# Optimization experiments

Hardware: AMD Instinct MI355X
Metric: run time of the kernel (lower is better)

The kernel has to match this reference:

```python
import jax, jax.numpy as jnp
import numpy as np

FEAT_DIM = 2048
H_DIM = 1024
N = 8192  # num_obj (tree nodes in pre-order traversal order)


def setup_inputs() -> dict:
    key = jax.random.key(0)
    ks = jax.random.split(key, 5)
    features = jax.random.normal(ks[0], (N, FEAT_DIM), dtype=jnp.float32)
    # block_orthogonal init approximated by scaled gaussian (same math at runtime)
    Wx = jax.random.normal(ks[1], (4 * H_DIM, FEAT_DIM), dtype=jnp.float32) / np.sqrt(FEAT_DIM)
    Wh = jax.random.normal(ks[2], (4 * H_DIM, H_DIM), dtype=jnp.float32) / np.sqrt(H_DIM)
    bx = jnp.zeros((4 * H_DIM,), dtype=jnp.float32)
    # iofuh bias: forget-gate block [2h:3h] filled with 1.0
    bh = jnp.zeros((4 * H_DIM,), dtype=jnp.float32).at[2 * H_DIM:3 * H_DIM].set(1.0)
    # binary tree in pre-order-compatible (topological) order: parent of t is (t-1)//2 < t; root = -1
    t = jnp.arange(N)
    parent_idx = jnp.where(t == 0, -1, (t - 1) // 2).astype(jnp.int32)
    root_c = jax.random.normal(ks[3], (1, H_DIM), dtype=jnp.float32)
    root_h = jax.random.normal(ks[4], (1, H_DIM), dtype=jnp.float32)
    return {"features": features, "Wx": Wx, "bx": bx, "Wh": Wh, "bh": bh,
            "parent_idx": parent_idx, "root_c": root_c, "root_h": root_h}


def reference(features, Wx, bx, Wh, bh, parent_idx, root_c, root_h):
    # Precompute the input projection for ALL nodes with one big GEMM
    # (the original does this per-node; math is identical).
    xproj = features @ Wx.T + (bx + bh)  # [N, 4H]
    WhT = Wh.T  # [H, 4H]
    # state buffers; slot 0 holds the root state, slot t+1 holds node t's state
    h_buf = jnp.concatenate([root_h, jnp.zeros((N, H_DIM), features.dtype)], axis=0)  # [N+1, H]
    c_buf = jnp.concatenate([root_c, jnp.zeros((N, H_DIM), features.dtype)], axis=0)

    def step(carry, inp):
        h_buf, c_buf = carry
        t, p, xp = inp
        hp = h_buf[p + 1]  # parent hidden [H]
        cp = c_buf[p + 1]  # parent cell   [H]
        iofu = xp + hp @ WhT  # [4H]
        i, o, f, u = jnp.split(iofu, 4)
        i = jax.nn.sigmoid(i)
        o = jax.nn.sigmoid(o)
        f = jax.nn.sigmoid(f)
        u = jnp.tanh(u)
        c = i * u + f * cp
        h = o * jnp.tanh(c)
        h_buf = h_buf.at[t + 1].set(h)
        c_buf = c_buf.at[t + 1].set(c)
        return (h_buf, c_buf), h

    ts = jnp.arange(N)
    (_, _), hidden = jax.lax.scan(step, (h_buf, c_buf), (ts, parent_idx, xproj))
    return hidden  # [N, H] == treelstm_io.hidden rows in traversal order
```

## Files before the change

kernel.cpp:

```cpp
#include <hip/hip_runtime.h>
#include <math.h>

#define FEAT 2048
#define HD 1024
#define FH 4096
#define NN 8192

using s16x8 = __attribute__((ext_vector_type(8))) short;
using f32x4 = __attribute__((ext_vector_type(4))) float;

#define GLOBAL_AS __attribute__((address_space(1)))
#define LDS_AS __attribute__((address_space(3)))

__device__ __forceinline__ void gload_lds16(const void* g, void* l) {
    __builtin_amdgcn_global_load_lds((const GLOBAL_AS unsigned int*)g,
                                     (LDS_AS unsigned int*)l, 16, 0, 0);
}

__device__ __forceinline__ unsigned short f2bf(float f) {
    union { float f; unsigned u; } v; v.f = f;
    unsigned r = v.u + 0x7FFFu + ((v.u >> 16) & 1u);
    return (unsigned short)(r >> 16);
}

__device__ __forceinline__ float fast_sig(float x) { return 1.0f / (1.0f + __expf(-x)); }
__device__ __forceinline__ float fast_tanh(float x) {
    float ax = fabsf(x);
    float e = __expf(2.0f * ax);
    float r = 1.0f - 2.0f / (e + 1.0f);
    return copysignf(r, x);
}

__global__ __launch_bounds__(256) void convert_all_kernel(
    const float* __restrict__ feat, const float* __restrict__ Wx,
    const float* __restrict__ Wh, unsigned short* __restrict__ feat_b,
    unsigned short* __restrict__ Wx_b, unsigned short* __restrict__ Wh_b)
{
    const size_t n1 = (size_t)NN * FEAT;
    const size_t n2 = n1 + (size_t)FH * FEAT;
    size_t i = ((size_t)blockIdx.x * 256 + threadIdx.x) * 8;
    const float* s; unsigned short* d;
    if (i < n1)      { s = feat + i;        d = feat_b + i; }
    else if (i < n2) { s = Wx + (i - n1);   d = Wx_b + (i - n1); }
    else             { s = Wh + (i - n2);   d = Wh_b + (i - n2); }
    float4 a = *(const float4*)s;
    float4 b = *(const float4*)(s + 4);
    unsigned short r[8] = {f2bf(a.x), f2bf(a.y), f2bf(a.z), f2bf(a.w),
                           f2bf(b.x), f2bf(b.y), f2bf(b.z), f2bf(b.w)};
    *(s16x8*)d = *(const s16x8*)r;
}

__global__ __launch_bounds__(256) void init_kernel(
    const float* __restrict__ root_h, const float* __restrict__ root_c,
    unsigned short* __restrict__ h_buf, float* __restrict__ c_buf)
{
    const int i = blockIdx.x * 256 + threadIdx.x;
    if (i < HD) { h_buf[i] = f2bf(root_h[i]); c_buf[i] = root_c[i]; }
}

__global__ __launch_bounds__(512, 2) void xproj_8ph(
    const unsigned short* __restrict__ Ab,
    const unsigned short* __restrict__ Bb,
    const float* __restrict__ bx, const float* __restrict__ bh,
    float* __restrict__ xproj)
{
    __shared__ char lds[131072];
    const int tid = threadIdx.x;
    const int wid = tid >> 6;
    const int lane = tid & 63;
    const int wr = wid >> 2;
    const int wc = wid & 3;
    const int bm = blockIdx.x * 256;
    const int bn = blockIdx.y * 256;
    const int fr = lane & 15;
    const int fq = lane >> 4;

    const int srow = tid >> 3;
    const int sslot = (tid & 7) ^ (srow & 7);
    const unsigned short* gA[4];
    const unsigned short* gB[4];
    #pragma unroll
    for (int q = 0; q < 4; ++q) {
        gA[q] = Ab + (size_t)(bm + q * 64 + srow) * FEAT + sslot * 8;
        gB[q] = Bb + (size_t)(bn + q * 64 + srow) * FEAT + sslot * 8;
    }
    const int ldsoff = tid * 16;

    f32x4 acc[8][4];
    #pragma unroll
    for (int i = 0; i < 8; ++i)
        #pragma unroll
        for (int j = 0; j < 4; ++j) { f32x4 z = {0.f, 0.f, 0.f, 0.f}; acc[i][j] = z; }

    #pragma unroll
    for (int q = 0; q < 4; ++q) {
        gload_lds16(gA[q], lds + q * 8192 + ldsoff);
        gload_lds16(gB[q], lds + 32768 + q * 8192 + ldsoff);
    }

    for (int t = 0; t < 32; ++t) {
        const int d = t & 1;
        const char* LA = lds + d * 65536;
        const char* LB = LA + 32768;
        char* SA = lds + (d ^ 1) * 65536;
        char* SB = SA + 32768;
        const int knext = (t + 1) * 64;

        asm volatile("s_waitcnt vmcnt(0)" ::: "memory");
        __builtin_amdgcn_s_barrier();

        #pragma unroll
        for (int kk = 0; kk < 2; ++kk) {
            const int kbyte = kk * 64 + fq * 16;
            s16x8 aF[8], bF[4];
            #pragma unroll
            for (int i = 0; i < 8; ++i) {
                const int row = wr * 128 + i * 16 + fr;
                aF[i] = *(const s16x8*)(LA + row * 128 + (kbyte ^ ((row & 7) << 4)));
            }
            #pragma unroll
            for (int j = 0; j < 4; ++j) {
                const int row = wc * 64 + j * 16 + fr;
                bF[j] = *(const s16x8*)(LB + row * 128 + (kbyte ^ ((row & 7) << 4)));
            }
            if (t < 31) {
                if (kk == 0) {
                    #pragma unroll
                    for (int q = 0; q < 4; ++q)
                        gload_lds16(gA[q] + knext, SA + q * 8192 + ldsoff);
                } else {
                    #pragma unroll
                    for (int q = 0; q < 4; ++q)
                        gload_lds16(gB[q] + knext, SB + q * 8192 + ldsoff);
                }
            }
            __builtin_amdgcn_s_setprio(1);
            #pragma unroll
            for (int i = 0; i < 8; ++i)
                #pragma unroll
                for (int j = 0; j < 4; ++j)
                    acc[i][j] = __builtin_amdgcn_mfma_f32_16x16x32_bf16(
                        aF[i], bF[j], acc[i][j], 0, 0, 0);
            __builtin_amdgcn_s_setprio(0);
        }
    }

    #pragma unroll
    for (int j = 0; j < 4; ++j) {
        const int col = bn + wc * 64 + j * 16 + fr;
        const float bias = bx[col] + bh[col];
        #pragma unroll
        for (int i = 0; i < 8; ++i) {
            const int rowb = bm + wr * 128 + i * 16 + fq * 4;
            #pragma unroll
            for (int reg = 0; reg < 4; ++reg)
                xproj[(size_t)(rowb + reg) * FH + col] = acc[i][j][reg] + bias;
        }
    }
}

template<int BM>
__global__ __launch_bounds__(512, 2) void level_kk(
    const float* __restrict__ xproj, const unsigned short* __restrict__ Whb,
    int start, int prevstart, unsigned short* __restrict__ h_buf,
    float* __restrict__ c_buf, float* __restrict__ out)
{
    constexpr int MR = BM / 32;
    constexpr int ABYTES = BM * 128;
    constexpr int BUF = ABYTES + 32768;
    __shared__ char lds[2 * BUF];
    const int tid = threadIdx.x;
    const int wid = tid >> 6, lane = tid & 63;
    const int wr = wid >> 2, wc = wid & 3;
    const int fr = lane & 15, fq = lane >> 4;
    const int t0 = start + blockIdx.x * BM;
    const int jg0 = blockIdx.y * 64;

    const int srow = tid >> 3;
    const int sslot = (tid & 7) ^ (srow & 7);
    const unsigned short* gA[BM / 64];
    #pragma unroll
    for (int q = 0; q < BM / 64; ++q) {
        const int rg = blockIdx.x * BM + q * 64 + srow;
        gA[q] = h_buf + (size_t)(prevstart + (rg >> 1) + 1) * HD + sslot * 8;
    }
    const unsigned short* gB[4];
    #pragma unroll
    for (int q = 0; q < 4; ++q) {
        const int r = q * 64 + srow;
        const int whrow = ((r >> 4) & 3) * 1024 + jg0 + ((r >> 6) * 16) + (r & 15);
        gB[q] = Whb + (size_t)whrow * HD + sslot * 8;
    }
    const int ldsoff = tid * 16;

    f32x4 acc[MR][4];
    #pragma unroll
    for (int i = 0; i < MR; ++i)
        #pragma unroll
        for (int j = 0; j < 4; ++j) { f32x4 z = {0.f, 0.f, 0.f, 0.f}; acc[i][j] = z; }

    #pragma unroll
    for (int q = 0; q < BM / 64; ++q)
        gload_lds16(gA[q], lds + q * 8192 + ldsoff);
    #pragma unroll
    for (int q = 0; q < 4; ++q)
        gload_lds16(gB[q], lds + ABYTES + q * 8192 + ldsoff);

    for (int t = 0; t < 16; ++t) {
        const char* LA = lds + (t & 1) * BUF;
        const char* LB = LA + ABYTES;
        char* SA = lds + ((t & 1) ^ 1) * BUF;
        char* SB = SA + ABYTES;
        const int knext = (t + 1) * 64;

        asm volatile("s_waitcnt vmcnt(0)" ::: "memory");
        __builtin_amdgcn_s_barrier();

        #pragma unroll
        for (int kk = 0; kk < 2; ++kk) {
            const int kbyte = kk * 64 + fq * 16;
            s16x8 aF[MR], bF[4];
            #pragma unroll
            for (int i = 0; i < MR; ++i) {
                const int row = wr * (BM / 2) + i * 16 + fr;
                aF[i] = *(const s16x8*)(LA + row * 128 + (kbyte ^ ((row & 7) << 4)));
            }
            #pragma unroll
            for (int j = 0; j < 4; ++j) {
                const int row = wc * 64 + j * 16 + fr;
                bF[j] = *(const s16x8*)(LB + row * 128 + (kbyte ^ ((row & 7) << 4)));
            }
            if (t < 15) {
                if (kk == 0) {
                    #pragma unroll
                    for (int q = 0; q < BM / 64; ++q)
                        gload_lds16(gA[q] + knext, SA + q * 8192 + ldsoff);
                } else {
                    #pragma unroll
                    for (int q = 0; q < 4; ++q)
                        gload_lds16(gB[q] + knext, SB + q * 8192 + ldsoff);
                }
            }
            __builtin_amdgcn_s_setprio(1);
            #pragma unroll
            for (int i = 0; i < MR; ++i)
                #pragma unroll
                for (int j = 0; j < 4; ++j)
                    acc[i][j] = __builtin_amdgcn_mfma_f32_16x16x32_bf16(
                        aF[i], bF[j], acc[i][j], 0, 0, 0);
            __builtin_amdgcn_s_setprio(0);
        }
    }

    const int col = jg0 + wc * 16 + fr;
    #pragma unroll
    for (int i = 0; i < MR; ++i) {
        #pragma unroll
        for (int reg = 0; reg < 4; ++reg) {
            const int t = t0 + wr * (BM / 2) + i * 16 + fq * 4 + reg;
            const int p = (t - 1) >> 1;
            const size_t xb = (size_t)t * FH + col;
            const float gi = acc[i][0][reg] + xproj[xb];
            const float go = acc[i][1][reg] + xproj[xb + HD];
            const float gf = acc[i][2][reg] + xproj[xb + 2 * HD];
            const float gu = acc[i][3][reg] + xproj[xb + 3 * HD];
            const float cp = c_buf[(size_t)(p + 1) * HD + col];
            const float c = fast_sig(gi) * fast_tanh(gu) + fast_sig(gf) * cp;
            const float h = fast_sig(go) * fast_tanh(c);
            c_buf[(size_t)(t + 1) * HD + col] = c;
            h_buf[(size_t)(t + 1) * HD + col] = f2bf(h);
            out[(size_t)t * HD + col] = h;
        }
    }
}

__device__ __forceinline__ void level_epilogue(
    f32x4 (&acc)[4][4], const float* __restrict__ xproj,
    const int* __restrict__ parent, unsigned short* __restrict__ h_buf,
    float* __restrict__ c_buf, float* __restrict__ out,
    int t0, int lim, int wm, int col, int fq)
{
    #pragma unroll
    for (int i = 0; i < 4; ++i) {
        #pragma unroll
        for (int reg = 0; reg < 4; ++reg) {
            const int t = t0 + wm + i * 16 + fq * 4 + reg;
            if (t < lim) {
                const int p = parent[t];
                const size_t xb = (size_t)t * FH + col;
                const float gi = acc[i][0][reg] + xproj[xb];
                const float go = acc[i][1][reg] + xproj[xb + HD];
                const float gf = acc[i][2][reg] + xproj[xb + 2 * HD];
                const float gu = acc[i][3][reg] + xproj[xb + 3 * HD];
                const float cp = c_buf[(size_t)(p + 1) * HD + col];
                const float c = fast_sig(gi) * fast_tanh(gu) + fast_sig(gf) * cp;
                const float h = fast_sig(go) * fast_tanh(c);
                c_buf[(size_t)(t + 1) * HD + col] = c;
                h_buf[(size_t)(t + 1) * HD + col] = f2bf(h);
                out[(size_t)t * HD + col] = h;
            }
        }
    }
}

__device__ __forceinline__ void bk128_issue(
    const unsigned short* const (&gA)[8], const unsigned short* const (&gB)[8],
    int k0, unsigned short* As, unsigned short* Bs, int wbase)
{
    #pragma unroll
    for (int q = 0; q < 8; ++q) {
        gload_lds16(gA[q] + k0, (char*)As + q * 4096 + wbase);
        gload_lds16(gB[q] + k0, (char*)Bs + q * 4096 + wbase);
    }
}

__device__ __forceinline__ void bk128_compute(
    const unsigned short* As, const unsigned short* Bs,
    f32x4 (&acc)[4][4], int wm, int wn16, int fr, int fkb)
{
    #pragma unroll
    for (int kk = 0; kk < 4; ++kk) {
        s16x8 aF[4], bF[4];
        #pragma unroll
        for (int i = 0; i < 4; ++i) {
            const int r = wm + i * 16 + fr;
            const int byteIn = (kk * 64 + fkb) ^ ((r & 7) << 4);
            aF[i] = *(const s16x8*)((const char*)As + r * 256 + byteIn);
        }
        #pragma unroll
        for (int g = 0; g < 4; ++g) {
            const int r = g * 32 + wn16 + fr;
            const int byteIn = (kk * 64 + fkb) ^ ((r & 7) << 4);
            bF[g] = *(const s16x8*)((const char*)Bs + r * 256 + byteIn);
        }
        #pragma unroll
        for (int i = 0; i < 4; ++i)
            #pragma unroll
            for (int g = 0; g < 4; ++g)
                acc[i][g] = __builtin_amdgcn_mfma_f32_16x16x32_bf16(aF[i], bF[g], acc[i][g], 0, 0, 0);
    }
}

__global__ __launch_bounds__(256) void level_bk128_dbuf(
    const float* __restrict__ xproj, const unsigned short* __restrict__ Whb,
    const int* __restrict__ parent, unsigned short* __restrict__ h_buf,
    float* __restrict__ c_buf, float* __restrict__ out,
    int start, int count)
{
    __shared__ unsigned short As0[128 * 128];
    __shared__ unsigned short Bs0[128 * 128];
    __shared__ unsigned short As1[128 * 128];
    __shared__ unsigned short Bs1[128 * 128];
    const int tid = threadIdx.x;
    const int wid = tid >> 6;
    const int lane = tid & 63;
    const int t0 = start + blockIdx.x * 128;
    const int jg0 = blockIdx.y * 32;
    const int lim = start + count;
    const int wm = (wid & 1) * 64;
    const int wn16 = (wid >> 1) * 16;
    const int wbase = wid * 1024;
    const int srow_b = tid >> 4;
    const int rowbyte = (tid & 15) * 16;

    const unsigned short* gA[8];
    const unsigned short* gB[8];
    #pragma unroll
    for (int q = 0; q < 8; ++q) {
        const int r = q * 16 + srow_b;
        const int sk = (rowbyte ^ ((r & 7) << 4)) >> 1;
        const int tA = min(t0 + r, lim - 1);
        gA[q] = h_buf + (size_t)(parent[tA] + 1) * HD + sk;
        const int whrow = ((r >> 5) << 10) + jg0 + (r & 31);
        gB[q] = Whb + (size_t)whrow * HD + sk;
    }

    f32x4 acc[4][4];
    #pragma unroll
    for (int i = 0; i < 4; ++i)
        #pragma unroll
        for (int g = 0; g < 4; ++g) { f32x4 z = {0.f, 0.f, 0.f, 0.f}; acc[i][g] = z; }

    const int fr = lane & 15;
    const int fkb = (lane >> 4) * 16;

    bk128_issue(gA, gB, 0, As0, Bs0, wbase);
    #pragma unroll
    for (int t = 0; t < 8; ++t) {
        unsigned short* curA = (t & 1) ? As1 : As0;
        unsigned short* curB = (t & 1) ? Bs1 : Bs0;
        unsigned short* nxtA = (t & 1) ? As0 : As1;
        unsigned short* nxtB = (t & 1) ? Bs0 : Bs1;
        if (t < 7) {
            bk128_issue(gA, gB, (t + 1) * 128, nxtA, nxtB, wbase);
            asm volatile("s_waitcnt vmcnt(16)" ::: "memory");
        } else {
            asm volatile("s_waitcnt vmcnt(0)" ::: "memory");
        }
        __builtin_amdgcn_s_barrier();
        __builtin_amdgcn_sched_barrier(0);
        bk128_compute(curA, curB, acc, wm, wn16, fr, fkb);
        __builtin_amdgcn_sched_barrier(0);
        __builtin_amdgcn_s_barrier();
    }

    level_epilogue(acc, xproj, parent, h_buf, c_buf, out,
                   t0, lim, wm, jg0 + wn16 + fr, lane >> 4);
}

extern "C" void kernel_launch(void* const* d_in, const int* in_sizes, int n_in,
                              void* d_out, int out_size, void* d_ws, size_t ws_size,
                              hipStream_t stream) {
    const float* feat   = (const float*)d_in[0];
    const float* Wx     = (const float*)d_in[1];
    const float* bx     = (const float*)d_in[2];
    const float* Wh     = (const float*)d_in[3];
    const float* bh     = (const float*)d_in[4];
    const int*   parent = (const int*)d_in[5];
    const float* root_c = (const float*)d_in[6];
    const float* root_h = (const float*)d_in[7];
    float* out = (float*)d_out;

    char* ws = (char*)d_ws;
    float* xproj = (float*)ws;                          ws += (size_t)NN * FH * 4;
    float* c_buf = (float*)ws;                          ws += (size_t)(NN + 1) * HD * 4;
    unsigned short* feat_b = (unsigned short*)ws;       ws += (size_t)NN * FEAT * 2;
    unsigned short* Wx_b = (unsigned short*)ws;         ws += (size_t)FH * FEAT * 2;
    unsigned short* Wh_b = (unsigned short*)ws;         ws += (size_t)FH * HD * 2;
    unsigned short* h_buf = (unsigned short*)ws;        ws += (size_t)(NN + 1) * HD * 2;

    const size_t ntot = (size_t)NN * FEAT + (size_t)FH * FEAT + (size_t)FH * HD;
    convert_all_kernel<<<(unsigned)(ntot / 8 / 256), 256, 0, stream>>>(
        feat, Wx, Wh, feat_b, Wx_b, Wh_b);
    init_kernel<<<4, 256, 0, stream>>>(root_h, root_c, h_buf, c_buf);

    dim3 g1(NN / 256, FH / 256);
    xproj_8ph<<<g1, 512, 0, stream>>>(feat_b, Wx_b, bx, bh, xproj);

    for (int start = 0, sz = 1; sz <= 512; start += sz, sz *= 2) {
        dim3 g2((sz + 127) / 128, HD / 32);
        level_bk128_dbuf<<<g2, 256, 0, stream>>>(
            xproj, Wh_b, parent, h_buf, c_buf, out, start, sz);
    }

    dim3 gl(16, 16);
    level_kk<64><<<gl, 512, 0, stream>>>(xproj, Wh_b, 1023, 511,
                                         h_buf, c_buf, out);
    level_kk<128><<<gl, 512, 0, stream>>>(xproj, Wh_b, 2047, 1023,
                                          h_buf, c_buf, out);
    level_kk<256><<<gl, 512, 0, stream>>>(xproj, Wh_b, 4095, 2047,
                                          h_buf, c_buf, out);

    dim3 g3(1, HD / 32);
    level_bk128_dbuf<<<g3, 256, 0, stream>>>(
        xproj, Wh_b, parent, h_buf, c_buf, out, 8191, 1);
}
```

Before: 463.0 us.

## Halve K-tile to BK=32 with new LDS swizzle and double level-kernel grid

Cuts the K-step of the xproj GEMM and the level GEMMs from 64 to 32, halving LDS per block, and raises the launch bound to 4 blocks per CU. The LDS layout changes to pack two 32-element rows per 128-byte line with an XOR swizzle. The level kernels shrink BM and double the grid in M, so the deep tree levels get more blocks. In exchange there are twice as many barrier and wait iterations, and asking for 4 blocks of 512 threads may force register spills given the large accumulator arrays.

```diff
diff --git a/kernel.cpp b/kernel.cpp
--- a/kernel.cpp
+++ b/kernel.cpp
@@ -58,13 +58,13 @@
     if (i < HD) { h_buf[i] = f2bf(root_h[i]); c_buf[i] = root_c[i]; }
 }
 
-__global__ __launch_bounds__(512, 2) void xproj_8ph(
+__global__ __launch_bounds__(512, 4) void xproj_8ph(
     const unsigned short* __restrict__ Ab,
     const unsigned short* __restrict__ Bb,
     const float* __restrict__ bx, const float* __restrict__ bh,
     float* __restrict__ xproj)
 {
-    __shared__ char lds[131072];
+    __shared__ char lds[65536];
     const int tid = threadIdx.x;
     const int wid = tid >> 6;
     const int lane = tid & 63;
@@ -75,14 +75,17 @@
     const int fr = lane & 15;
     const int fq = lane >> 4;
 
-    const int srow = tid >> 3;
-    const int sslot = (tid & 7) ^ (srow & 7);
-    const unsigned short* gA[4];
-    const unsigned short* gB[4];
-    #pragma unroll
-    for (int q = 0; q < 4; ++q) {
-        gA[q] = Ab + (size_t)(bm + q * 64 + srow) * FEAT + sslot * 8;
-        gB[q] = Bb + (size_t)(bn + q * 64 + srow) * FEAT + sslot * 8;
+    const int sR = tid >> 3;
+    const int ss = tid & 7;
+    const unsigned short* gA[2];
+    const unsigned short* gB[2];
+    #pragma unroll
+    for (int q = 0; q < 2; ++q) {
+        const int R = q * 64 + sR;
+        const int node = 2 * R + (ss & 1);
+        const int ck = (ss >> 1) ^ (R & 3);
+        gA[q] = Ab + (size_t)(bm + node) * FEAT + ck * 8;
+        gB[q] = Bb + (size_t)(bn + node) * FEAT + ck * 8;
     }
     const int ldsoff = tid * 16;
 
@@ -93,56 +96,51 @@
         for (int j = 0; j < 4; ++j) { f32x4 z = {0.f, 0.f, 0.f, 0.f}; acc[i][j] = z; }
 
     #pragma unroll
-    for (int q = 0; q < 4; ++q) {
+    for (int q = 0; q < 2; ++q) {
         gload_lds16(gA[q], lds + q * 8192 + ldsoff);
-        gload_lds16(gB[q], lds + 32768 + q * 8192 + ldsoff);
-    }
-
-    for (int t = 0; t < 32; ++t) {
-        const int d = t & 1;
-        const char* LA = lds + d * 65536;
-        const char* LB = LA + 32768;
-        char* SA = lds + (d ^ 1) * 65536;
-        char* SB = SA + 32768;
-        const int knext = (t + 1) * 64;
+        gload_lds16(gB[q], lds + 16384 + q * 8192 + ldsoff);
+    }
+
+    for (int t = 0; t < 64; ++t) {
+        const char* LA = lds + (t & 1) * 32768;
+        const char* LB = LA + 16384;
+        char* SA = lds + ((t & 1) ^ 1) * 32768;
+        char* SB = SA + 16384;
+        const int knext = (t + 1) * 32;
 
         asm volatile("s_waitcnt vmcnt(0)" ::: "memory");
         __builtin_amdgcn_s_barrier();
 
-        #pragma unroll
-        for (int kk = 0; kk < 2; ++kk) {
-            const int kbyte = kk * 64 + fq * 16;
-            s16x8 aF[8], bF[4];
-            #pragma unroll
-            for (int i = 0; i < 8; ++i) {
-                const int row = wr * 128 + i * 16 + fr;
-                aF[i] = *(const s16x8*)(LA + row * 128 + (kbyte ^ ((row & 7) << 4)));
+        s16x8 aF[8], bF[4];
+        #pragma unroll
+        for (int i = 0; i < 8; ++i) {
+            const int r = wr * 128 + i * 16 + fr;
+            const int R = r >> 1;
+            const int s = ((fq ^ (R & 3)) << 1) | (r & 1);
+            aF[i] = *(const s16x8*)(LA + R * 128 + s * 16);
+        }
+        #pragma unroll
+        for (int j = 0; j < 4; ++j) {
+            const int r = wc * 64 + j * 16 + fr;
+            const int R = r >> 1;
+            const int s = ((fq ^ (R & 3)) << 1) | (r & 1);
+            bF[j] = *(const s16x8*)(LB + R * 128 + s * 16);
+        }
+        if (t < 63) {
+            #pragma unroll
+            for (int q = 0; q < 2; ++q) {
+                gload_lds16(gA[q] + knext, SA + q * 8192 + ldsoff);
+                gload_lds16(gB[q] + knext, SB + q * 8192 + ldsoff);
             }
-            #pragma unroll
-            for (int j = 0; j < 4; ++j) {
-                const int row = wc * 64 + j * 16 + fr;
-                bF[j] = *(const s16x8*)(LB + row * 128 + (kbyte ^ ((row & 7) << 4)));
-            }
-            if (t < 31) {
-                if (kk == 0) {
-                    #pragma unroll
-                    for (int q = 0; q < 4; ++q)
-                        gload_lds16(gA[q] + knext, SA + q * 8192 + ldsoff);
-                } else {
-                    #pragma unroll
-                    for (int q = 0; q < 4; ++q)
-                        gload_lds16(gB[q] + knext, SB + q * 8192 + ldsoff);
-                }
-            }
-            __builtin_amdgcn_s_setprio(1);
-            #pragma unroll
-            for (int i = 0; i < 8; ++i)
-                #pragma unroll
-                for (int j = 0; j < 4; ++j)
-                    acc[i][j] = __builtin_amdgcn_mfma_f32_16x16x32_bf16(
-                        aF[i], bF[j], acc[i][j], 0, 0, 0);
-            __builtin_amdgcn_s_setprio(0);
-        }
+        }
+        __builtin_amdgcn_s_setprio(1);
+        #pragma unroll
+        for (int i = 0; i < 8; ++i)
+            #pragma unroll
+            for (int j = 0; j < 4; ++j)
+                acc[i][j] = __builtin_amdgcn_mfma_f32_16x16x32_bf16(
+                    aF[i], bF[j], acc[i][j], 0, 0, 0);
+        __builtin_amdgcn_s_setprio(0);
     }
 
     #pragma unroll
@@ -160,14 +158,14 @@
 }
 
 template<int BM>
-__global__ __launch_bounds__(512, 2) void level_kk(
+__global__ __launch_bounds__(512, 4) void level_kk(
     const float* __restrict__ xproj, const unsigned short* __restrict__ Whb,
     int start, int prevstart, unsigned short* __restrict__ h_buf,
     float* __restrict__ c_buf, float* __restrict__ out)
 {
     constexpr int MR = BM / 32;
-    constexpr int ABYTES = BM * 128;
-    constexpr int BUF = ABYTES + 32768;
+    constexpr int ABYTES = BM * 64;
+    constexpr int BUF = ABYTES + 16384;
     __shared__ char lds[2 * BUF];
     const int tid = threadIdx.x;
     const int wid = tid >> 6, lane = tid & 63;
@@ -176,20 +174,19 @@
     const int t0 = start + blockIdx.x * BM;
     const int jg0 = blockIdx.y * 64;
 
-    const int srow = tid >> 3;
-    const int sslot = (tid & 7) ^ (srow & 7);
-    const unsigned short* gA[BM / 64];
-    #pragma unroll
-    for (int q = 0; q < BM / 64; ++q) {
-        const int rg = blockIdx.x * BM + q * 64 + srow;
-        gA[q] = h_buf + (size_t)(prevstart + (rg >> 1) + 1) * HD + sslot * 8;
-    }
-    const unsigned short* gB[4];
-    #pragma unroll
-    for (int q = 0; q < 4; ++q) {
-        const int r = q * 64 + srow;
-        const int whrow = ((r >> 4) & 3) * 1024 + jg0 + ((r >> 6) * 16) + (r & 15);
-        gB[q] = Whb + (size_t)whrow * HD + sslot * 8;
+    const int sR = tid >> 3;
+    const int ss = tid & 7;
+    const bool aAct = (tid < BM * 4);
+    const unsigned short* gA0 = h_buf +
+        (size_t)(prevstart + blockIdx.x * (BM / 2) + sR + 1) * HD +
+        ((ss >> 1) ^ (sR & 3)) * 8;
+    const unsigned short* gB[2];
+    #pragma unroll
+    for (int q = 0; q < 2; ++q) {
+        const int R = q * 64 + sR;
+        const int br = 2 * R + (ss & 1);
+        const int whrow = ((br >> 4) & 3) * 1024 + jg0 + ((br >> 6) * 16) + (br & 15);
+        gB[q] = Whb + (size_t)whrow * HD + ((ss >> 1) ^ (R & 3)) * 8;
     }
     const int ldsoff = tid * 16;
 
@@ -199,57 +196,50 @@
         #pragma unroll
         for (int j = 0; j < 4; ++j) { f32x4 z = {0.f, 0.f, 0.f, 0.f}; acc[i][j] = z; }
 
-    #pragma unroll
-    for (int q = 0; q < BM / 64; ++q)
-        gload_lds16(gA[q], lds + q * 8192 + ldsoff);
-    #pragma unroll
-    for (int q = 0; q < 4; ++q)
+    if (aAct) gload_lds16(gA0, lds + ldsoff);
+    #pragma unroll
+    for (int q = 0; q < 2; ++q)
         gload_lds16(gB[q], lds + ABYTES + q * 8192 + ldsoff);
 
-    for (int t = 0; t < 16; ++t) {
+    for (int t = 0; t < 32; ++t) {
         const char* LA = lds + (t & 1) * BUF;
         const char* LB = LA + ABYTES;
         char* SA = lds + ((t & 1) ^ 1) * BUF;
         char* SB = SA + ABYTES;
-        const int knext = (t + 1) * 64;
+        const int knext = (t + 1) * 32;
 
         asm volatile("s_waitcnt vmcnt(0)" ::: "memory");
         __builtin_amdgcn_s_barrier();
 
-        #pragma unroll
-        for (int kk = 0; kk < 2; ++kk) {
-            const int kbyte = kk * 64 + fq * 16;
-            s16x8 aF[MR], bF[4];
-            #pragma unroll
-            for (int i = 0; i < MR; ++i) {
-                const int row = wr * (BM / 2) + i * 16 + fr;
-                aF[i] = *(const s16x8*)(LA + row * 128 + (kbyte ^ ((row & 7) << 4)));
-            }
-            #pragma unroll
-            for (int j = 0; j < 4; ++j) {
-                const int row = wc * 64 + j * 16 + fr;
-                bF[j] = *(const s16x8*)(LB + row * 128 + (kbyte ^ ((row & 7) << 4)));
-            }
-            if (t < 15) {
-                if (kk == 0) {
-                    #pragma unroll
-                    for (int q = 0; q < BM / 64; ++q)
-                        gload_lds16(gA[q] + knext, SA + q * 8192 + ldsoff);
-                } else {
-                    #pragma unroll
-                    for (int q = 0; q < 4; ++q)
-                        gload_lds16(gB[q] + knext, SB + q * 8192 + ldsoff);
-                }
-            }
-            __builtin_amdgcn_s_setprio(1);
-            #pragma unroll
-            for (int i = 0; i < MR; ++i)
-                #pragma unroll
-                for (int j = 0; j < 4; ++j)
-                    acc[i][j] = __builtin_amdgcn_mfma_f32_16x16x32_bf16(
-                        aF[i], bF[j], acc[i][j], 0, 0, 0);
-            __builtin_amdgcn_s_setprio(0);
-        }
+        s16x8 aF[MR], bF[4];
+        #pragma unroll
+        for (int i = 0; i < MR; ++i) {
+            const int r = wr * (BM / 2) + i * 16 + fr;
+            const int R = r >> 1;
+            const int s = ((fq ^ (R & 3)) << 1) | (r & 1);
+            aF[i] = *(const s16x8*)(LA + R * 128 + s * 16);
+        }
+        #pragma unroll
+        for (int j = 0; j < 4; ++j) {
+            const int r = wc * 64 + j * 16 + fr;
+            const int R = r >> 1;
+            const int s = ((fq ^ (R & 3)) << 1) | (r & 1);
+            bF[j] = *(const s16x8*)(LB + R * 128 + s * 16);
+        }
+        if (t < 31) {
+            if (aAct) gload_lds16(gA0 + knext, SA + ldsoff);
+            #pragma unroll
+            for (int q = 0; q < 2; ++q)
+                gload_lds16(gB[q] + knext, SB + q * 8192 + ldsoff);
+        }
+        __builtin_amdgcn_s_setprio(1);
+        #pragma unroll
+        for (int i = 0; i < MR; ++i)
+            #pragma unroll
+            for (int j = 0; j < 4; ++j)
+                acc[i][j] = __builtin_amdgcn_mfma_f32_16x16x32_bf16(
+                    aF[i], bF[j], acc[i][j], 0, 0, 0);
+        __builtin_amdgcn_s_setprio(0);
     }
 
     const int col = jg0 + wc * 16 + fr;
@@ -443,12 +433,12 @@
             xproj, Wh_b, parent, h_buf, c_buf, out, start, sz);
     }
 
-    dim3 gl(16, 16);
-    level_kk<64><<<gl, 512, 0, stream>>>(xproj, Wh_b, 1023, 511,
+    dim3 gl(32, 16);
+    level_kk<32><<<gl, 512, 0, stream>>>(xproj, Wh_b, 1023, 511,
                                          h_buf, c_buf, out);
-    level_kk<128><<<gl, 512, 0, stream>>>(xproj, Wh_b, 2047, 1023,
-                                          h_buf, c_buf, out);
-    level_kk<256><<<gl, 512, 0, stream>>>(xproj, Wh_b, 4095, 2047,
+    level_kk<64><<<gl, 512, 0, stream>>>(xproj, Wh_b, 2047, 1023,
+                                         h_buf, c_buf, out);
+    level_kk<128><<<gl, 512, 0, stream>>>(xproj, Wh_b, 4095, 2047,
                                           h_buf, c_buf, out);
 
     dim3 g3(1, HD / 32);
```

New measurement: 1.624 ms. 251% more time.

## Switch xproj GEMM to 3-stage LDS pipeline with K=32 tiles

Applied to the files above, without the earlier changes.

The xproj GEMM now streams K in 32-wide chunks through a triple-buffered LDS ring (96KB instead of 128KB), using a partial vmcnt wait so two loads stay in flight while computing. Each LDS row packs two matrix rows, with a new XOR swizzle adapted to the half-width chunks. The goal is to hide global-load latency better and lower LDS footprint, at the cost of twice as many barriers per K and smaller MFMA batches per barrier. The out index change is arithmetically identical.

```diff
diff --git a/kernel.cpp b/kernel.cpp
--- a/kernel.cpp
+++ b/kernel.cpp
@@ -64,7 +64,7 @@
     const float* __restrict__ bx, const float* __restrict__ bh,
     float* __restrict__ xproj)
 {
-    __shared__ char lds[131072];
+    __shared__ char lds[98304];
     const int tid = threadIdx.x;
     const int wid = tid >> 6;
     const int lane = tid & 63;
@@ -75,14 +75,17 @@
     const int fr = lane & 15;
     const int fq = lane >> 4;
 
-    const int srow = tid >> 3;
-    const int sslot = (tid & 7) ^ (srow & 7);
-    const unsigned short* gA[4];
-    const unsigned short* gB[4];
-    #pragma unroll
-    for (int q = 0; q < 4; ++q) {
-        gA[q] = Ab + (size_t)(bm + q * 64 + srow) * FEAT + sslot * 8;
-        gB[q] = Bb + (size_t)(bn + q * 64 + srow) * FEAT + sslot * 8;
+    const int sR = tid >> 3;
+    const int ss = tid & 7;
+    const unsigned short* gA[2];
+    const unsigned short* gB[2];
+    #pragma unroll
+    for (int q = 0; q < 2; ++q) {
+        const int R = q * 64 + sR;
+        const int node = 2 * R + (ss & 1);
+        const int ck = (ss >> 1) ^ (R & 3);
+        gA[q] = Ab + (size_t)(bm + node) * FEAT + ck * 8;
+        gB[q] = Bb + (size_t)(bn + node) * FEAT + ck * 8;
     }
     const int ldsoff = tid * 16;
 
@@ -93,56 +96,59 @@
         for (int j = 0; j < 4; ++j) { f32x4 z = {0.f, 0.f, 0.f, 0.f}; acc[i][j] = z; }
 
     #pragma unroll
-    for (int q = 0; q < 4; ++q) {
-        gload_lds16(gA[q], lds + q * 8192 + ldsoff);
-        gload_lds16(gB[q], lds + 32768 + q * 8192 + ldsoff);
-    }
-
-    for (int t = 0; t < 32; ++t) {
-        const int d = t & 1;
-        const char* LA = lds + d * 65536;
-        const char* LB = LA + 32768;
-        char* SA = lds + (d ^ 1) * 65536;
-        char* SB = SA + 32768;
-        const int knext = (t + 1) * 64;
-
-        asm volatile("s_waitcnt vmcnt(0)" ::: "memory");
+    for (int t = 0; t < 2; ++t) {
+        char* S = lds + t * 32768;
+        #pragma unroll
+        for (int q = 0; q < 2; ++q) {
+            gload_lds16(gA[q] + t * 32, S + q * 8192 + ldsoff);
+            gload_lds16(gB[q] + t * 32, S + 16384 + q * 8192 + ldsoff);
+        }
+    }
+
+    int cur = 0;
+    for (int t = 0; t < 64; ++t) {
+        const char* LA = lds + cur * 32768;
+        const char* LB = LA + 16384;
+
+        if (t < 63) { asm volatile("s_waitcnt vmcnt(4)" ::: "memory"); }
+        else        { asm volatile("s_waitcnt vmcnt(0)" ::: "memory"); }
         __builtin_amdgcn_s_barrier();
 
-        #pragma unroll
-        for (int kk = 0; kk < 2; ++kk) {
-            const int kbyte = kk * 64 + fq * 16;
-            s16x8 aF[8], bF[4];
-            #pragma unroll
-            for (int i = 0; i < 8; ++i) {
-                const int row = wr * 128 + i * 16 + fr;
-                aF[i] = *(const s16x8*)(LA + row * 128 + (kbyte ^ ((row & 7) << 4)));
+        if (t < 62) {
+            char* S = lds + ((cur + 2) % 3) * 32768;
+            const int knext = (t + 2) * 32;
+            #pragma unroll
+            for (int q = 0; q < 2; ++q) {
+                gload_lds16(gA[q] + knext, S + q * 8192 + ldsoff);
+                gload_lds16(gB[q] + knext, S + 16384 + q * 8192 + ldsoff);
             }
-            #pragma unroll
-            for (int j = 0; j < 4; ++j) {
-                const int row = wc * 64 + j * 16 + fr;
-                bF[j] = *(const s16x8*)(LB + row * 128 + (kbyte ^ ((row & 7) << 4)));
-            }
-            if (t < 31) {
-                if (kk == 0) {
-                    #pragma unroll
-                    for (int q = 0; q < 4; ++q)
-                        gload_lds16(gA[q] + knext, SA + q * 8192 + ldsoff);
-                } else {
-                    #pragma unroll
-                    for (int q = 0; q < 4; ++q)
-                        gload_lds16(gB[q] + knext, SB + q * 8192 + ldsoff);
-                }
-            }
-            __builtin_amdgcn_s_setprio(1);
-            #pragma unroll
-            for (int i = 0; i < 8; ++i)
-                #pragma unroll
-                for (int j = 0; j < 4; ++j)
-                    acc[i][j] = __builtin_amdgcn_mfma_f32_16x16x32_bf16(
-                        aF[i], bF[j], acc[i][j], 0, 0, 0);
-            __builtin_amdgcn_s_setprio(0);
-        }
+        }
+
+        s16x8 aF[8], bF[4];
+        #pragma unroll
+        for (int i = 0; i < 8; ++i) {
+            const int r = wr * 128 + i * 16 + fr;
+            const int R = r >> 1;
+            const int s = ((fq ^ (R & 3)) << 1) | (r & 1);
+            aF[i] = *(const s16x8*)(LA + R * 128 + s * 16);
+        }
+        #pragma unroll
+        for (int j = 0; j < 4; ++j) {
+            const int r = wc * 64 + j * 16 + fr;
+            const int R = r >> 1;
+            const int s = ((fq ^ (R & 3)) << 1) | (r & 1);
+            bF[j] = *(const s16x8*)(LB + R * 128 + s * 16);
+        }
+        __builtin_amdgcn_s_setprio(1);
+        #pragma unroll
+        for (int i = 0; i < 8; ++i)
+            #pragma unroll
+            for (int j = 0; j < 4; ++j)
+                acc[i][j] = __builtin_amdgcn_mfma_f32_16x16x32_bf16(
+                    aF[i], bF[j], acc[i][j], 0, 0, 0);
+        __builtin_amdgcn_s_setprio(0);
+
+        cur = (cur + 1) % 3;
     }
 
     #pragma unroll
@@ -269,7 +275,7 @@
             const float h = fast_sig(go) * fast_tanh(c);
             c_buf[(size_t)(t + 1) * HD + col] = c;
             h_buf[(size_t)(t + 1) * HD + col] = f2bf(h);
-            out[(size_t)t * HD + col] = h;
+            out[(size_t)t * FH / 4 + col] = h;
         }
     }
 }
```

New measurement: 469.3 us. No clear change (+1.4%).
